# Performance work log

Measured on AMD Instinct MI355X. Metric: run time of the kernel, lower is better.

## Reference

```python
import jax, jax.numpy as jnp
import numpy as np

MAX_STEPS = 50
B, H, A = 4096, 1024, 128


def setup_inputs() -> dict:
    key = jax.random.key(0)
    ks = jax.random.split(key, 7)
    s = 1.0 / np.sqrt(H)  # torch default LSTM/Linear init scale
    return {
        "encoder_output": jax.random.normal(ks[0], (1, B, H), dtype=jnp.float32),
        "w_ih": jax.random.normal(ks[1], (4 * H, H), dtype=jnp.float32) * s,
        "w_hh": jax.random.normal(ks[2], (4 * H, H), dtype=jnp.float32) * s,
        "b_ih": jax.random.normal(ks[3], (4 * H,), dtype=jnp.float32) * s,
        "b_hh": jax.random.normal(ks[4], (4 * H,), dtype=jnp.float32) * s,
        "w_pred": jax.random.normal(ks[5], (A, H), dtype=jnp.float32) * s,
        "b_pred": jax.random.normal(ks[6], (A,), dtype=jnp.float32) * s,
    }


def reference(encoder_output, w_ih, w_hh, b_ih, b_hh, w_pred, b_pred):
    # LSTM output (hidden state) of step t; seq_len is always 1.
    hidden = w_hh.shape[1]
    x0 = encoder_output[0]                        # (B, H)
    h0 = jnp.zeros_like(x0)
    c0 = jnp.zeros_like(x0)
    bias = b_ih + b_hh                            # (4H,)

    def step(carry, _):
        x, h, c = carry
        gates = x @ w_ih.T + h @ w_hh.T + bias    # (B, 4H)
        i, f, g, o = jnp.split(gates, 4, axis=-1)  # torch gate order i,f,g,o
        c_new = jax.nn.sigmoid(f) * c + jax.nn.sigmoid(i) * jnp.tanh(g)
        h_new = jax.nn.sigmoid(o) * jnp.tanh(c_new)
        p = h_new @ w_pred.T + b_pred             # (B, A)
        return (h_new, h_new, c_new), p

    _, predicted = jax.lax.scan(step, (x0, h0, c0), None, length=MAX_STEPS)
    return predicted  # (MAX_STEPS, B, A)
```

## Files before the change

kernel.cpp:

```cpp
#include <hip/hip_runtime.h>
#include <hip/hip_bf16.h>
#include <stdint.h>


#define B_SZ   4096
#define H_SZ   1024
#define A_SZ   128
#define NSTEP  50
#define NT     16

using bf16 = __hip_bfloat16;
typedef __attribute__((ext_vector_type(8))) short bf16x8;
typedef __attribute__((ext_vector_type(4))) float f32x4;

__device__ __forceinline__ void gload_lds16(const void* g, void* l) {
    __builtin_amdgcn_global_load_lds(
        (const __attribute__((address_space(1))) unsigned int*)g,
        (__attribute__((address_space(3))) unsigned int*)l, 16, 0, 0);
}

#define FENCE() asm volatile("" ::: "memory")
#define BAR()   do { FENCE(); __builtin_amdgcn_s_barrier(); FENCE(); } while (0)
#define VMC6()  asm volatile("s_waitcnt vmcnt(6)" ::: "memory")
#define VMC0()  asm volatile("s_waitcnt vmcnt(0)" ::: "memory")
#define LGKM0() asm volatile("s_waitcnt lgkmcnt(0)" ::: "memory")

__device__ __forceinline__ float sigf(float x) {
    return 1.f / (1.f + __expf(-x));
}
__device__ __forceinline__ float tanh_(float x) {
    float e = __expf(-2.f * fabsf(x));
    float t = (1.f - e) / (1.f + e);
    return copysignf(t, x);
}


__global__ void prep_weights(const float4* __restrict__ wih,
                             const float4* __restrict__ whh,
                             bf16* __restrict__ Wc, bf16* __restrict__ Wi) {
    int i = blockIdx.x * 256 + threadIdx.x;
    float4 a = wih[i], b = whh[i];
    bf16 tc[4] = {__float2bfloat16(a.x + b.x), __float2bfloat16(a.y + b.y),
                  __float2bfloat16(a.z + b.z), __float2bfloat16(a.w + b.w)};
    bf16 ti[4] = {__float2bfloat16(a.x), __float2bfloat16(a.y),
                  __float2bfloat16(a.z), __float2bfloat16(a.w)};
    *(uint64_t*)(Wc + 4 * (size_t)i) = *(const uint64_t*)tc;
    *(uint64_t*)(Wi + 4 * (size_t)i) = *(const uint64_t*)ti;
}

__global__ void prep_cast(const float4* __restrict__ in, bf16* __restrict__ out) {
    int i = blockIdx.x * 256 + threadIdx.x;
    float4 a = in[i];
    bf16 t[4] = {__float2bfloat16(a.x), __float2bfloat16(a.y),
                 __float2bfloat16(a.z), __float2bfloat16(a.w)};
    *(uint64_t*)(out + 4 * (size_t)i) = *(const uint64_t*)t;
}

__global__ void prep_bias(const float* __restrict__ a, const float* __restrict__ b,
                          float* __restrict__ o) {
    int i = blockIdx.x * 256 + threadIdx.x;
    o[i] = a[i] + b[i];
}


__global__ __launch_bounds__(512, 2)
void lstm_gates(const bf16* __restrict__ hin, const bf16* __restrict__ W,
                const float* __restrict__ bias, float* __restrict__ c,
                bf16* __restrict__ hout, int step0) {
    __shared__ __align__(16) bf16 sm[65536];
    bf16* const lA0 = sm;
    bf16* const lA1 = sm + 16384;
    bf16* const lB0 = sm + 32768;
    bf16* const lB1 = sm + 49152;

    const int tid  = threadIdx.x;
    const int w    = tid >> 6;
    const int lane = tid & 63;
    const int wr   = w >> 2;
    const int wc   = w & 3;

    const int bid     = blockIdx.x;
    const int logical = (bid & 7) * 32 + (bid >> 3);
    const int bm0     = (logical >> 4) * 256;
    const int j0      = (logical & 15) * 64;

    const int scolb = ((tid & 7) * 16) ^ (((tid >> 3) & 7) << 4);
    const char* baseA = (const char*)hin + (size_t)(bm0 + (tid >> 3)) * 2048 + scolb;
    const char* baseB = (const char*)W   + (size_t)(j0  + (tid >> 3)) * 2048 + scolb;

    const int cs0 = ((      (lane >> 4) * 16) ^ ((lane & 7) << 4)) >> 1;
    const int cs1 = ((64 + (lane >> 4) * 16) ^ ((lane & 7) << 4)) >> 1;
    const int rA  = (wr * 128 + (lane & 15)) * 64;
    const int rB  = (wc * 16  + (lane & 15)) * 64;

    f32x4 acc[8][4];
    const f32x4 z = {0.f, 0.f, 0.f, 0.f};
#pragma unroll
    for (int m = 0; m < 8; ++m)
#pragma unroll
        for (int n = 0; n < 4; ++n) acc[m][n] = z;

    auto SGA = [&](int t, int h) {
        bf16* dst = ((t & 1) ? lA1 : lA0) + h * 8192 + w * 512;
        const char* g = baseA + (size_t)(h * 128) * 2048 + (size_t)t * 128;
        gload_lds16(g, dst);
        gload_lds16(g + (size_t)64 * 2048, dst + 4096);
    };
    auto SGB = [&](int t, int h) {
        bf16* dst = ((t & 1) ? lB1 : lB0) + h * 8192 + w * 512;
        const char* g = baseB + (size_t)(h * 2) * 2097152 + (size_t)t * 128;
        gload_lds16(g, dst);
        gload_lds16(g + 2097152, dst + 4096);
    };

    SGB(0, 0); SGB(0, 1); SGA(0, 0); SGA(0, 1);
    SGB(1, 0); SGB(1, 1); SGA(1, 0);
    VMC6();
    BAR();

    for (int t = 0; t < NT; ++t) {
        const bf16* Ad = (t & 1) ? lA1 : lA0;
        const bf16* Bd = (t & 1) ? lB1 : lB0;
        bf16x8 av[4][2], bv[4][2];

#pragma unroll
        for (int m = 0; m < 4; ++m) {
            av[m][0] = *(const bf16x8*)(Ad + rA + m * 1024 + cs0);
            av[m][1] = *(const bf16x8*)(Ad + rA + m * 1024 + cs1);
        }
#pragma unroll
        for (int n = 0; n < 2; ++n) {
            bv[n][0] = *(const bf16x8*)(Bd + rB + n * 4096 + cs0);
            bv[n][1] = *(const bf16x8*)(Bd + rB + n * 4096 + cs1);
        }
        if (t + 1 < NT) SGA(t + 1, 1);
        BAR(); LGKM0();
        __builtin_amdgcn_s_setprio(1);
#pragma unroll
        for (int n = 0; n < 2; ++n)
#pragma unroll
            for (int m = 0; m < 4; ++m) {
                acc[m][n] = __builtin_amdgcn_mfma_f32_16x16x32_bf16(av[m][0], bv[n][0], acc[m][n], 0, 0, 0);
                acc[m][n] = __builtin_amdgcn_mfma_f32_16x16x32_bf16(av[m][1], bv[n][1], acc[m][n], 0, 0, 0);
            }
        __builtin_amdgcn_s_setprio(0);
        BAR();

#pragma unroll
        for (int n = 2; n < 4; ++n) {
            bv[n][0] = *(const bf16x8*)(Bd + rB + n * 4096 + cs0);
            bv[n][1] = *(const bf16x8*)(Bd + rB + n * 4096 + cs1);
        }
        if (t + 2 < NT) SGB(t + 2, 0);
        BAR(); LGKM0();
        __builtin_amdgcn_s_setprio(1);
#pragma unroll
        for (int n = 2; n < 4; ++n)
#pragma unroll
            for (int m = 0; m < 4; ++m) {
                acc[m][n] = __builtin_amdgcn_mfma_f32_16x16x32_bf16(av[m][0], bv[n][0], acc[m][n], 0, 0, 0);
                acc[m][n] = __builtin_amdgcn_mfma_f32_16x16x32_bf16(av[m][1], bv[n][1], acc[m][n], 0, 0, 0);
            }
        __builtin_amdgcn_s_setprio(0);
        BAR();

#pragma unroll
        for (int m = 0; m < 4; ++m) {
            av[m][0] = *(const bf16x8*)(Ad + rA + (m + 4) * 1024 + cs0);
            av[m][1] = *(const bf16x8*)(Ad + rA + (m + 4) * 1024 + cs1);
        }
        if (t + 2 < NT) SGB(t + 2, 1);
        BAR(); LGKM0();
        __builtin_amdgcn_s_setprio(1);
#pragma unroll
        for (int n = 0; n < 2; ++n)
#pragma unroll
            for (int m = 0; m < 4; ++m) {
                acc[m + 4][n] = __builtin_amdgcn_mfma_f32_16x16x32_bf16(av[m][0], bv[n][0], acc[m + 4][n], 0, 0, 0);
                acc[m + 4][n] = __builtin_amdgcn_mfma_f32_16x16x32_bf16(av[m][1], bv[n][1], acc[m + 4][n], 0, 0, 0);
            }
        __builtin_amdgcn_s_setprio(0);
        BAR();

        if (t + 2 < NT) SGA(t + 2, 0);
        BAR(); LGKM0();
        __builtin_amdgcn_s_setprio(1);
#pragma unroll
        for (int n = 2; n < 4; ++n)
#pragma unroll
            for (int m = 0; m < 4; ++m) {
                acc[m + 4][n] = __builtin_amdgcn_mfma_f32_16x16x32_bf16(av[m][0], bv[n][0], acc[m + 4][n], 0, 0, 0);
                acc[m + 4][n] = __builtin_amdgcn_mfma_f32_16x16x32_bf16(av[m][1], bv[n][1], acc[m + 4][n], 0, 0, 0);
            }
        __builtin_amdgcn_s_setprio(0);
        if (t < NT - 1) {
            if (t == NT - 2) { VMC0(); } else { VMC6(); }
        }
        BAR();
    }

    const int jc = j0 + wc * 16 + (lane & 15);
    const float bi  = bias[jc];
    const float bff = bias[H_SZ + jc];
    const float bg  = bias[2 * H_SZ + jc];
    const float bo  = bias[3 * H_SZ + jc];
#pragma unroll
    for (int m = 0; m < 8; ++m) {
#pragma unroll
        for (int r = 0; r < 4; ++r) {
            int row = bm0 + wr * 128 + m * 16 + (lane >> 4) * 4 + r;
            size_t idx = (size_t)row * H_SZ + jc;
            float iv = acc[m][0][r] + bi;
            float fv = acc[m][1][r] + bff;
            float gv = acc[m][2][r] + bg;
            float ov = acc[m][3][r] + bo;
            float cp = step0 ? 0.f : c[idx];
            float cn = sigf(fv) * cp + sigf(iv) * tanh_(gv);
            float hn = sigf(ov) * tanh_(cn);
            c[idx] = cn;
            hout[idx] = __float2bfloat16(hn);
        }
    }
}


__global__ __launch_bounds__(256)
void pred_kernel(const bf16* __restrict__ h, const bf16* __restrict__ wp,
                 const float* __restrict__ bp, float* __restrict__ out) {
    __shared__ __align__(16) bf16 lH[16 * 64];
    __shared__ __align__(16) bf16 lP[128 * 64];

    const int tid  = threadIdx.x;
    const int w    = tid >> 6;
    const int lane = tid & 63;
    const int bm0  = blockIdx.x * 16;

    const int scolb = ((tid & 7) * 16) ^ (((tid >> 3) & 7) << 4);
    const int cs0 = ((      (lane >> 4) * 16) ^ ((lane & 7) << 4)) >> 1;
    const int cs1 = ((64 + (lane >> 4) * 16) ^ ((lane & 7) << 4)) >> 1;

    f32x4 acc[2];
    const f32x4 z = {0.f, 0.f, 0.f, 0.f};
    acc[0] = z; acc[1] = z;

    const char* hb = (const char*)h  + (size_t)(bm0 + (tid >> 3)) * 2048 + scolb;
    const char* pb = (const char*)wp + (size_t)(tid >> 3) * 2048 + scolb;

    for (int t = 0; t < NT; ++t) {
        __syncthreads();
        if (tid < 128)
            gload_lds16(hb + (size_t)t * 128, lH + w * 512);
#pragma unroll
        for (int q = 0; q < 4; ++q)
            gload_lds16(pb + (size_t)(q * 32) * 2048 + (size_t)t * 128,
                        lP + (q * 4 + w) * 512);
        __syncthreads();

        bf16x8 a0 = *(const bf16x8*)(lH + (lane & 15) * 64 + cs0);
        bf16x8 a1 = *(const bf16x8*)(lH + (lane & 15) * 64 + cs1);
#pragma unroll
        for (int n = 0; n < 2; ++n) {
            int rowb = (w * 32 + n * 16 + (lane & 15)) * 64;
            bf16x8 b0 = *(const bf16x8*)(lP + rowb + cs0);
            bf16x8 b1 = *(const bf16x8*)(lP + rowb + cs1);
            acc[n] = __builtin_amdgcn_mfma_f32_16x16x32_bf16(a0, b0, acc[n], 0, 0, 0);
            acc[n] = __builtin_amdgcn_mfma_f32_16x16x32_bf16(a1, b1, acc[n], 0, 0, 0);
        }
    }

#pragma unroll
    for (int n = 0; n < 2; ++n)
#pragma unroll
        for (int r = 0; r < 4; ++r) {
            int row = bm0 + (lane >> 4) * 4 + r;
            int col = w * 32 + n * 16 + (lane & 15);
            out[(size_t)row * A_SZ + col] = acc[n][r] + bp[col];
        }
}


extern "C" void kernel_launch(void* const* d_in, const int* in_sizes, int n_in,
                              void* d_out, int out_size, void* d_ws, size_t ws_size,
                              hipStream_t stream) {
    const float* enc   = (const float*)d_in[0];
    const float* wih   = (const float*)d_in[1];
    const float* whh   = (const float*)d_in[2];
    const float* bih   = (const float*)d_in[3];
    const float* bhh   = (const float*)d_in[4];
    const float* wpred = (const float*)d_in[5];
    const float* bpred = (const float*)d_in[6];
    float* out = (float*)d_out;

    char* ws = (char*)d_ws;
    const size_t WH = (size_t)4 * H_SZ * H_SZ;
    const size_t BH = (size_t)B_SZ * H_SZ;
    bf16*  Wc   = (bf16*)ws;                 ws += WH * 2;
    bf16*  Wi   = (bf16*)ws;                 ws += WH * 2;
    bf16*  h0   = (bf16*)ws;                 ws += BH * 2;
    bf16*  h1   = (bf16*)ws;                 ws += BH * 2;
    float* cbuf = (float*)ws;                ws += BH * 4;
    bf16*  wp   = (bf16*)ws;                 ws += (size_t)A_SZ * H_SZ * 2;
    float* bias = (float*)ws;                ws += 4 * H_SZ * 4;

    prep_weights<<<4096, 256, 0, stream>>>((const float4*)wih, (const float4*)whh, Wc, Wi);
    prep_cast<<<128, 256, 0, stream>>>((const float4*)wpred, wp);
    prep_bias<<<16, 256, 0, stream>>>(bih, bhh, bias);
    prep_cast<<<4096, 256, 0, stream>>>((const float4*)enc, h0);

    bf16* hbuf[2] = {h0, h1};
    for (int s = 0; s < NSTEP; ++s) {
        const bf16* hin = hbuf[s & 1];
        bf16* hout      = hbuf[(s + 1) & 1];
        lstm_gates<<<256, 512, 0, stream>>>(
            hin, (s == 0) ? Wi : Wc, bias, cbuf, hout, s == 0 ? 1 : 0);
        pred_kernel<<<256, 256, 0, stream>>>(
            hout, wp, bpred, out + (size_t)s * B_SZ * A_SZ);
    }
}
```

Before: 2.671 ms.

## Fuse all LSTM steps and prediction into one persistent cooperative kernel

Replaces the 100 per-step launches (gates kernel plus prediction kernel) with a single cooperative kernel that loops over all 50 steps and uses grid.sync between steps. The cell state now stays in registers instead of being read from and written to global memory every step. The prediction GEMM is folded into the same kernel after the sync and reads h and w_pred straight from global memory. The next step's first tile loads are issued before the prediction work so the two can overlap. In exchange, every step now pays a grid-wide barrier, the whole grid of 256 blocks must be co-resident, and the longer-lived state raises register pressure.

```diff
diff --git a/kernel.cpp b/kernel.cpp
--- a/kernel.cpp
+++ b/kernel.cpp
@@ -1,6 +1,9 @@
 #include <hip/hip_runtime.h>
 #include <hip/hip_bf16.h>
+#include <hip/hip_cooperative_groups.h>
 #include <stdint.h>
+
+namespace cg = cooperative_groups;
 
 
 #define B_SZ   4096
@@ -64,20 +67,24 @@
 
 
 __global__ __launch_bounds__(512, 2)
-void lstm_gates(const bf16* __restrict__ hin, const bf16* __restrict__ W,
-                const float* __restrict__ bias, float* __restrict__ c,
-                bf16* __restrict__ hout, int step0) {
+void lstm_persist(const bf16* __restrict__ Wc, const bf16* __restrict__ Wi,
+                  bf16* __restrict__ hA, bf16* __restrict__ hB,
+                  const float* __restrict__ bias, const bf16* __restrict__ wp,
+                  const float* __restrict__ bp, float* __restrict__ out) {
+    cg::grid_group grid = cg::this_grid();
     __shared__ __align__(16) bf16 sm[65536];
     bf16* const lA0 = sm;
     bf16* const lA1 = sm + 16384;
     bf16* const lB0 = sm + 32768;
     bf16* const lB1 = sm + 49152;
 
-    const int tid  = threadIdx.x;
-    const int w    = tid >> 6;
-    const int lane = tid & 63;
-    const int wr   = w >> 2;
-    const int wc   = w & 3;
+    const int tid    = threadIdx.x;
+    const int w      = tid >> 6;
+    const int lane   = tid & 63;
+    const int wr     = w >> 2;
+    const int wc     = w & 3;
+    const int lane15 = lane & 15;
+    const int lhi    = lane >> 4;
 
     const int bid     = blockIdx.x;
     const int logical = (bid & 7) * 32 + (bid >> 3);
@@ -85,197 +92,181 @@
     const int j0      = (logical & 15) * 64;
 
     const int scolb = ((tid & 7) * 16) ^ (((tid >> 3) & 7) << 4);
-    const char* baseA = (const char*)hin + (size_t)(bm0 + (tid >> 3)) * 2048 + scolb;
-    const char* baseB = (const char*)W   + (size_t)(j0  + (tid >> 3)) * 2048 + scolb;
-
-    const int cs0 = ((      (lane >> 4) * 16) ^ ((lane & 7) << 4)) >> 1;
-    const int cs1 = ((64 + (lane >> 4) * 16) ^ ((lane & 7) << 4)) >> 1;
-    const int rA  = (wr * 128 + (lane & 15)) * 64;
-    const int rB  = (wc * 16  + (lane & 15)) * 64;
-
-    f32x4 acc[8][4];
-    const f32x4 z = {0.f, 0.f, 0.f, 0.f};
+    const size_t offA = (size_t)(bm0 + (tid >> 3)) * 2048 + scolb;
+    const size_t offB = (size_t)(j0  + (tid >> 3)) * 2048 + scolb;
+
+    const int cs0 = ((     lhi * 16) ^ ((lane & 7) << 4)) >> 1;
+    const int cs1 = ((64 + lhi * 16) ^ ((lane & 7) << 4)) >> 1;
+    const int rA  = (wr * 128 + lane15) * 64;
+    const int rB  = (wc * 16  + lane15) * 64;
+
+    const int jc = j0 + wc * 16 + lane15;
+    const float bi  = bias[jc];
+    const float bff = bias[H_SZ + jc];
+    const float bg  = bias[2 * H_SZ + jc];
+    const float bo  = bias[3 * H_SZ + jc];
+    const float bpv = bp[w * 16 + lane15];
+    const int pr0 = logical * 16;
+
+    float creg[8][4];
 #pragma unroll
     for (int m = 0; m < 8; ++m)
 #pragma unroll
-        for (int n = 0; n < 4; ++n) acc[m][n] = z;
+        for (int r = 0; r < 4; ++r) creg[m][r] = 0.f;
+
+    const char* gA = (const char*)hA + offA;
+    const char* gB = (const char*)Wi + offB;
 
     auto SGA = [&](int t, int h) {
         bf16* dst = ((t & 1) ? lA1 : lA0) + h * 8192 + w * 512;
-        const char* g = baseA + (size_t)(h * 128) * 2048 + (size_t)t * 128;
+        const char* g = gA + (size_t)(h * 128) * 2048 + (size_t)t * 128;
         gload_lds16(g, dst);
         gload_lds16(g + (size_t)64 * 2048, dst + 4096);
     };
     auto SGB = [&](int t, int h) {
         bf16* dst = ((t & 1) ? lB1 : lB0) + h * 8192 + w * 512;
-        const char* g = baseB + (size_t)(h * 2) * 2097152 + (size_t)t * 128;
+        const char* g = gB + (size_t)(h * 2) * 2097152 + (size_t)t * 128;
         gload_lds16(g, dst);
         gload_lds16(g + 2097152, dst + 4096);
     };
 
     SGB(0, 0); SGB(0, 1); SGA(0, 0); SGA(0, 1);
     SGB(1, 0); SGB(1, 1); SGA(1, 0);
-    VMC6();
-    BAR();
-
-    for (int t = 0; t < NT; ++t) {
-        const bf16* Ad = (t & 1) ? lA1 : lA0;
-        const bf16* Bd = (t & 1) ? lB1 : lB0;
-        bf16x8 av[4][2], bv[4][2];
-
-#pragma unroll
-        for (int m = 0; m < 4; ++m) {
-            av[m][0] = *(const bf16x8*)(Ad + rA + m * 1024 + cs0);
-            av[m][1] = *(const bf16x8*)(Ad + rA + m * 1024 + cs1);
+
+    const f32x4 z = {0.f, 0.f, 0.f, 0.f};
+
+    for (int s = 0; s < NSTEP; ++s) {
+        bf16* hnew = (s & 1) ? hA : hB;
+
+        VMC6();
+        BAR();
+
+        f32x4 acc[8][4];
+#pragma unroll
+        for (int m = 0; m < 8; ++m)
+#pragma unroll
+            for (int n = 0; n < 4; ++n) acc[m][n] = z;
+
+        for (int t = 0; t < NT; ++t) {
+            const bf16* Ad = (t & 1) ? lA1 : lA0;
+            const bf16* Bd = (t & 1) ? lB1 : lB0;
+            bf16x8 av[4][2], bv[4][2];
+
+#pragma unroll
+            for (int m = 0; m < 4; ++m) {
+                av[m][0] = *(const bf16x8*)(Ad + rA + m * 1024 + cs0);
+                av[m][1] = *(const bf16x8*)(Ad + rA + m * 1024 + cs1);
+            }
+#pragma unroll
+            for (int n = 0; n < 2; ++n) {
+                bv[n][0] = *(const bf16x8*)(Bd + rB + n * 4096 + cs0);
+                bv[n][1] = *(const bf16x8*)(Bd + rB + n * 4096 + cs1);
+            }
+            if (t + 1 < NT) SGA(t + 1, 1);
+            BAR(); LGKM0();
+            __builtin_amdgcn_s_setprio(1);
+#pragma unroll
+            for (int n = 0; n < 2; ++n)
+#pragma unroll
+                for (int m = 0; m < 4; ++m) {
+                    acc[m][n] = __builtin_amdgcn_mfma_f32_16x16x32_bf16(av[m][0], bv[n][0], acc[m][n], 0, 0, 0);
+                    acc[m][n] = __builtin_amdgcn_mfma_f32_16x16x32_bf16(av[m][1], bv[n][1], acc[m][n], 0, 0, 0);
+                }
+            __builtin_amdgcn_s_setprio(0);
+            BAR();
+
+#pragma unroll
+            for (int n = 2; n < 4; ++n) {
+                bv[n][0] = *(const bf16x8*)(Bd + rB + n * 4096 + cs0);
+                bv[n][1] = *(const bf16x8*)(Bd + rB + n * 4096 + cs1);
+            }
+            if (t + 2 < NT) SGB(t + 2, 0);
+            BAR(); LGKM0();
+            __builtin_amdgcn_s_setprio(1);
+#pragma unroll
+            for (int n = 2; n < 4; ++n)
+#pragma unroll
+                for (int m = 0; m < 4; ++m) {
+                    acc[m][n] = __builtin_amdgcn_mfma_f32_16x16x32_bf16(av[m][0], bv[n][0], acc[m][n], 0, 0, 0);
+                    acc[m][n] = __builtin_amdgcn_mfma_f32_16x16x32_bf16(av[m][1], bv[n][1], acc[m][n], 0, 0, 0);
+                }
+            __builtin_amdgcn_s_setprio(0);
+            BAR();
+
+#pragma unroll
+            for (int m = 0; m < 4; ++m) {
+                av[m][0] = *(const bf16x8*)(Ad + rA + (m + 4) * 1024 + cs0);
+                av[m][1] = *(const bf16x8*)(Ad + rA + (m + 4) * 1024 + cs1);
+            }
+            if (t + 2 < NT) SGB(t + 2, 1);
+            BAR(); LGKM0();
+            __builtin_amdgcn_s_setprio(1);
+#pragma unroll
+            for (int n = 0; n < 2; ++n)
+#pragma unroll
+                for (int m = 0; m < 4; ++m) {
+                    acc[m + 4][n] = __builtin_amdgcn_mfma_f32_16x16x32_bf16(av[m][0], bv[n][0], acc[m + 4][n], 0, 0, 0);
+                    acc[m + 4][n] = __builtin_amdgcn_mfma_f32_16x16x32_bf16(av[m][1], bv[n][1], acc[m + 4][n], 0, 0, 0);
+                }
+            __builtin_amdgcn_s_setprio(0);
+            BAR();
+
+            if (t + 2 < NT) SGA(t + 2, 0);
+            BAR(); LGKM0();
+            __builtin_amdgcn_s_setprio(1);
+#pragma unroll
+            for (int n = 2; n < 4; ++n)
+#pragma unroll
+                for (int m = 0; m < 4; ++m) {
+                    acc[m + 4][n] = __builtin_amdgcn_mfma_f32_16x16x32_bf16(av[m][0], bv[n][0], acc[m + 4][n], 0, 0, 0);
+                    acc[m + 4][n] = __builtin_amdgcn_mfma_f32_16x16x32_bf16(av[m][1], bv[n][1], acc[m + 4][n], 0, 0, 0);
+                }
+            __builtin_amdgcn_s_setprio(0);
+            if (t < NT - 1) {
+                if (t == NT - 2) { VMC0(); } else { VMC6(); }
+            }
+            BAR();
         }
-#pragma unroll
-        for (int n = 0; n < 2; ++n) {
-            bv[n][0] = *(const bf16x8*)(Bd + rB + n * 4096 + cs0);
-            bv[n][1] = *(const bf16x8*)(Bd + rB + n * 4096 + cs1);
+
+#pragma unroll
+        for (int m = 0; m < 8; ++m) {
+#pragma unroll
+            for (int r = 0; r < 4; ++r) {
+                int row = bm0 + wr * 128 + m * 16 + lhi * 4 + r;
+                float iv = acc[m][0][r] + bi;
+                float fv = acc[m][1][r] + bff;
+                float gv = acc[m][2][r] + bg;
+                float ov = acc[m][3][r] + bo;
+                float cn = sigf(fv) * creg[m][r] + sigf(iv) * tanh_(gv);
+                float hn = sigf(ov) * tanh_(cn);
+                creg[m][r] = cn;
+                hnew[(size_t)row * H_SZ + jc] = __float2bfloat16(hn);
+            }
         }
-        if (t + 1 < NT) SGA(t + 1, 1);
-        BAR(); LGKM0();
-        __builtin_amdgcn_s_setprio(1);
-#pragma unroll
-        for (int n = 0; n < 2; ++n)
-#pragma unroll
-            for (int m = 0; m < 4; ++m) {
-                acc[m][n] = __builtin_amdgcn_mfma_f32_16x16x32_bf16(av[m][0], bv[n][0], acc[m][n], 0, 0, 0);
-                acc[m][n] = __builtin_amdgcn_mfma_f32_16x16x32_bf16(av[m][1], bv[n][1], acc[m][n], 0, 0, 0);
-            }
-        __builtin_amdgcn_s_setprio(0);
-        BAR();
-
-#pragma unroll
-        for (int n = 2; n < 4; ++n) {
-            bv[n][0] = *(const bf16x8*)(Bd + rB + n * 4096 + cs0);
-            bv[n][1] = *(const bf16x8*)(Bd + rB + n * 4096 + cs1);
+
+        grid.sync();
+
+        if (s + 1 < NSTEP) {
+            gA = (const char*)hnew + offA;
+            gB = (const char*)Wc + offB;
+            SGB(0, 0); SGB(0, 1); SGA(0, 0); SGA(0, 1);
+            SGB(1, 0); SGB(1, 1); SGA(1, 0);
         }
-        if (t + 2 < NT) SGB(t + 2, 0);
-        BAR(); LGKM0();
-        __builtin_amdgcn_s_setprio(1);
-#pragma unroll
-        for (int n = 2; n < 4; ++n)
-#pragma unroll
-            for (int m = 0; m < 4; ++m) {
-                acc[m][n] = __builtin_amdgcn_mfma_f32_16x16x32_bf16(av[m][0], bv[n][0], acc[m][n], 0, 0, 0);
-                acc[m][n] = __builtin_amdgcn_mfma_f32_16x16x32_bf16(av[m][1], bv[n][1], acc[m][n], 0, 0, 0);
-            }
-        __builtin_amdgcn_s_setprio(0);
-        BAR();
-
-#pragma unroll
-        for (int m = 0; m < 4; ++m) {
-            av[m][0] = *(const bf16x8*)(Ad + rA + (m + 4) * 1024 + cs0);
-            av[m][1] = *(const bf16x8*)(Ad + rA + (m + 4) * 1024 + cs1);
+
+        const bf16* hp  = hnew + (size_t)(pr0 + lane15) * H_SZ + lhi * 8;
+        const bf16* wpp = wp   + (size_t)(w * 16 + lane15) * H_SZ + lhi * 8;
+        f32x4 pacc = z;
+#pragma unroll 4
+        for (int ks = 0; ks < 32; ++ks) {
+            bf16x8 a = *(const bf16x8*)(hp + ks * 32);
+            bf16x8 b = *(const bf16x8*)(wpp + ks * 32);
+            pacc = __builtin_amdgcn_mfma_f32_16x16x32_bf16(a, b, pacc, 0, 0, 0);
         }
-        if (t + 2 < NT) SGB(t + 2, 1);
-        BAR(); LGKM0();
-        __builtin_amdgcn_s_setprio(1);
-#pragma unroll
-        for (int n = 0; n < 2; ++n)
-#pragma unroll
-            for (int m = 0; m < 4; ++m) {
-                acc[m + 4][n] = __builtin_amdgcn_mfma_f32_16x16x32_bf16(av[m][0], bv[n][0], acc[m + 4][n], 0, 0, 0);
-                acc[m + 4][n] = __builtin_amdgcn_mfma_f32_16x16x32_bf16(av[m][1], bv[n][1], acc[m + 4][n], 0, 0, 0);
-            }
-        __builtin_amdgcn_s_setprio(0);
-        BAR();
-
-        if (t + 2 < NT) SGA(t + 2, 0);
-        BAR(); LGKM0();
-        __builtin_amdgcn_s_setprio(1);
-#pragma unroll
-        for (int n = 2; n < 4; ++n)
-#pragma unroll
-            for (int m = 0; m < 4; ++m) {
-                acc[m + 4][n] = __builtin_amdgcn_mfma_f32_16x16x32_bf16(av[m][0], bv[n][0], acc[m + 4][n], 0, 0, 0);
-                acc[m + 4][n] = __builtin_amdgcn_mfma_f32_16x16x32_bf16(av[m][1], bv[n][1], acc[m + 4][n], 0, 0, 0);
-            }
-        __builtin_amdgcn_s_setprio(0);
-        if (t < NT - 1) {
-            if (t == NT - 2) { VMC0(); } else { VMC6(); }
-        }
-        BAR();
+        float* op = out + (size_t)s * (B_SZ * A_SZ)
+                  + (size_t)(pr0 + lhi * 4) * A_SZ + w * 16 + lane15;
+#pragma unroll
+        for (int r = 0; r < 4; ++r) op[r * A_SZ] = pacc[r] + bpv;
     }
-
-    const int jc = j0 + wc * 16 + (lane & 15);
-    const float bi  = bias[jc];
-    const float bff = bias[H_SZ + jc];
-    const float bg  = bias[2 * H_SZ + jc];
-    const float bo  = bias[3 * H_SZ + jc];
-#pragma unroll
-    for (int m = 0; m < 8; ++m) {
-#pragma unroll
-        for (int r = 0; r < 4; ++r) {
-            int row = bm0 + wr * 128 + m * 16 + (lane >> 4) * 4 + r;
-            size_t idx = (size_t)row * H_SZ + jc;
-            float iv = acc[m][0][r] + bi;
-            float fv = acc[m][1][r] + bff;
-            float gv = acc[m][2][r] + bg;
-            float ov = acc[m][3][r] + bo;
-            float cp = step0 ? 0.f : c[idx];
-            float cn = sigf(fv) * cp + sigf(iv) * tanh_(gv);
-            float hn = sigf(ov) * tanh_(cn);
-            c[idx] = cn;
-            hout[idx] = __float2bfloat16(hn);
-        }
-    }
-}
-
-
-__global__ __launch_bounds__(256)
-void pred_kernel(const bf16* __restrict__ h, const bf16* __restrict__ wp,
-                 const float* __restrict__ bp, float* __restrict__ out) {
-    __shared__ __align__(16) bf16 lH[16 * 64];
-    __shared__ __align__(16) bf16 lP[128 * 64];
-
-    const int tid  = threadIdx.x;
-    const int w    = tid >> 6;
-    const int lane = tid & 63;
-    const int bm0  = blockIdx.x * 16;
-
-    const int scolb = ((tid & 7) * 16) ^ (((tid >> 3) & 7) << 4);
-    const int cs0 = ((      (lane >> 4) * 16) ^ ((lane & 7) << 4)) >> 1;
-    const int cs1 = ((64 + (lane >> 4) * 16) ^ ((lane & 7) << 4)) >> 1;
-
-    f32x4 acc[2];
-    const f32x4 z = {0.f, 0.f, 0.f, 0.f};
-    acc[0] = z; acc[1] = z;
-
-    const char* hb = (const char*)h  + (size_t)(bm0 + (tid >> 3)) * 2048 + scolb;
-    const char* pb = (const char*)wp + (size_t)(tid >> 3) * 2048 + scolb;
-
-    for (int t = 0; t < NT; ++t) {
-        __syncthreads();
-        if (tid < 128)
-            gload_lds16(hb + (size_t)t * 128, lH + w * 512);
-#pragma unroll
-        for (int q = 0; q < 4; ++q)
-            gload_lds16(pb + (size_t)(q * 32) * 2048 + (size_t)t * 128,
-                        lP + (q * 4 + w) * 512);
-        __syncthreads();
-
-        bf16x8 a0 = *(const bf16x8*)(lH + (lane & 15) * 64 + cs0);
-        bf16x8 a1 = *(const bf16x8*)(lH + (lane & 15) * 64 + cs1);
-#pragma unroll
-        for (int n = 0; n < 2; ++n) {
-            int rowb = (w * 32 + n * 16 + (lane & 15)) * 64;
-            bf16x8 b0 = *(const bf16x8*)(lP + rowb + cs0);
-            bf16x8 b1 = *(const bf16x8*)(lP + rowb + cs1);
-            acc[n] = __builtin_amdgcn_mfma_f32_16x16x32_bf16(a0, b0, acc[n], 0, 0, 0);
-            acc[n] = __builtin_amdgcn_mfma_f32_16x16x32_bf16(a1, b1, acc[n], 0, 0, 0);
-        }
-    }
-
-#pragma unroll
-    for (int n = 0; n < 2; ++n)
-#pragma unroll
-        for (int r = 0; r < 4; ++r) {
-            int row = bm0 + (lane >> 4) * 4 + r;
-            int col = w * 32 + n * 16 + (lane & 15);
-            out[(size_t)row * A_SZ + col] = acc[n][r] + bp[col];
-        }
 }
 
 
@@ -298,7 +289,6 @@
     bf16*  Wi   = (bf16*)ws;                 ws += WH * 2;
     bf16*  h0   = (bf16*)ws;                 ws += BH * 2;
     bf16*  h1   = (bf16*)ws;                 ws += BH * 2;
-    float* cbuf = (float*)ws;                ws += BH * 4;
     bf16*  wp   = (bf16*)ws;                 ws += (size_t)A_SZ * H_SZ * 2;
     float* bias = (float*)ws;                ws += 4 * H_SZ * 4;
 
@@ -307,13 +297,8 @@
     prep_bias<<<16, 256, 0, stream>>>(bih, bhh, bias);
     prep_cast<<<4096, 256, 0, stream>>>((const float4*)enc, h0);
 
-    bf16* hbuf[2] = {h0, h1};
-    for (int s = 0; s < NSTEP; ++s) {
-        const bf16* hin = hbuf[s & 1];
-        bf16* hout      = hbuf[(s + 1) & 1];
-        lstm_gates<<<256, 512, 0, stream>>>(
-            hin, (s == 0) ? Wi : Wc, bias, cbuf, hout, s == 0 ? 1 : 0);
-        pred_kernel<<<256, 256, 0, stream>>>(
-            hout, wp, bpred, out + (size_t)s * B_SZ * A_SZ);
-    }
-}
+    void* args[] = {(void*)&Wc, (void*)&Wi, (void*)&h0, (void*)&h1,
+                    (void*)&bias, (void*)&wp, (void*)&bpred, (void*)&out};
+    hipLaunchCooperativeKernel((const void*)lstm_persist, dim3(256), dim3(512),
+                               args, 0, stream);
+}
```

Result: slower. 4.479 ms (+67.7%).

## Fuse prediction projection of previous step into next LSTM gates kernel

Applied to the files above, without the earlier changes.

The per-step prediction kernel is removed. Each lstm_gates launch now computes the output projection for the previous step's hidden state (its input hin) in its prologue, overlapping with the initial async LDS loads, and a single pred_kernel handles the final step. This halves the number of kernel launches and reuses the hidden-state read, at the cost of extra prologue work and register pressure in the gates kernel.

```diff
diff --git a/kernel.cpp b/kernel.cpp
--- a/kernel.cpp
+++ b/kernel.cpp
@@ -66,18 +66,22 @@
 __global__ __launch_bounds__(512, 2)
 void lstm_gates(const bf16* __restrict__ hin, const bf16* __restrict__ W,
                 const float* __restrict__ bias, float* __restrict__ c,
-                bf16* __restrict__ hout, int step0) {
+                bf16* __restrict__ hout, int step0,
+                const bf16* __restrict__ wp, const float* __restrict__ bp,
+                float* __restrict__ pout) {
     __shared__ __align__(16) bf16 sm[65536];
     bf16* const lA0 = sm;
     bf16* const lA1 = sm + 16384;
     bf16* const lB0 = sm + 32768;
     bf16* const lB1 = sm + 49152;
 
-    const int tid  = threadIdx.x;
-    const int w    = tid >> 6;
-    const int lane = tid & 63;
-    const int wr   = w >> 2;
-    const int wc   = w & 3;
+    const int tid    = threadIdx.x;
+    const int w      = tid >> 6;
+    const int lane   = tid & 63;
+    const int wr     = w >> 2;
+    const int wc     = w & 3;
+    const int lane15 = lane & 15;
+    const int lhi    = lane >> 4;
 
     const int bid     = blockIdx.x;
     const int logical = (bid & 7) * 32 + (bid >> 3);
@@ -88,10 +92,10 @@
     const char* baseA = (const char*)hin + (size_t)(bm0 + (tid >> 3)) * 2048 + scolb;
     const char* baseB = (const char*)W   + (size_t)(j0  + (tid >> 3)) * 2048 + scolb;
 
-    const int cs0 = ((      (lane >> 4) * 16) ^ ((lane & 7) << 4)) >> 1;
-    const int cs1 = ((64 + (lane >> 4) * 16) ^ ((lane & 7) << 4)) >> 1;
-    const int rA  = (wr * 128 + (lane & 15)) * 64;
-    const int rB  = (wc * 16  + (lane & 15)) * 64;
+    const int cs0 = ((     lhi * 16) ^ ((lane & 7) << 4)) >> 1;
+    const int cs1 = ((64 + lhi * 16) ^ ((lane & 7) << 4)) >> 1;
+    const int rA  = (wr * 128 + lane15) * 64;
+    const int rB  = (wc * 16  + lane15) * 64;
 
     f32x4 acc[8][4];
     const f32x4 z = {0.f, 0.f, 0.f, 0.f};
@@ -115,6 +119,24 @@
 
     SGB(0, 0); SGB(0, 1); SGA(0, 0); SGA(0, 1);
     SGB(1, 0); SGB(1, 1); SGA(1, 0);
+
+    if (pout) {
+        const int pr0 = logical * 16;
+        const bf16* hp  = hin + (size_t)(pr0 + lane15) * H_SZ + lhi * 8;
+        const bf16* wpp = wp  + (size_t)(w * 16 + lane15) * H_SZ + lhi * 8;
+        f32x4 pacc = z;
+#pragma unroll 4
+        for (int ks = 0; ks < 32; ++ks) {
+            bf16x8 a = *(const bf16x8*)(hp + ks * 32);
+            bf16x8 b = *(const bf16x8*)(wpp + ks * 32);
+            pacc = __builtin_amdgcn_mfma_f32_16x16x32_bf16(a, b, pacc, 0, 0, 0);
+        }
+        const float bpv = bp[w * 16 + lane15];
+        float* op = pout + (size_t)(pr0 + lhi * 4) * A_SZ + w * 16 + lane15;
+#pragma unroll
+        for (int r = 0; r < 4; ++r) op[r * A_SZ] = pacc[r] + bpv;
+    }
+
     VMC6();
     BAR();
 
@@ -199,7 +221,7 @@
         BAR();
     }
 
-    const int jc = j0 + wc * 16 + (lane & 15);
+    const int jc = j0 + wc * 16 + lane15;
     const float bi  = bias[jc];
     const float bff = bias[H_SZ + jc];
     const float bg  = bias[2 * H_SZ + jc];
@@ -208,7 +230,7 @@
     for (int m = 0; m < 8; ++m) {
 #pragma unroll
         for (int r = 0; r < 4; ++r) {
-            int row = bm0 + wr * 128 + m * 16 + (lane >> 4) * 4 + r;
+            int row = bm0 + wr * 128 + m * 16 + lhi * 4 + r;
             size_t idx = (size_t)row * H_SZ + jc;
             float iv = acc[m][0][r] + bi;
             float fv = acc[m][1][r] + bff;
@@ -311,9 +333,11 @@
     for (int s = 0; s < NSTEP; ++s) {
         const bf16* hin = hbuf[s & 1];
         bf16* hout      = hbuf[(s + 1) & 1];
+        float* pout = (s == 0) ? nullptr : out + (size_t)(s - 1) * (B_SZ * A_SZ);
         lstm_gates<<<256, 512, 0, stream>>>(
-            hin, (s == 0) ? Wi : Wc, bias, cbuf, hout, s == 0 ? 1 : 0);
-        pred_kernel<<<256, 256, 0, stream>>>(
-            hout, wp, bpred, out + (size_t)s * B_SZ * A_SZ);
-    }
-}
+            hin, (s == 0) ? Wi : Wc, bias, cbuf, hout, s == 0 ? 1 : 0,
+            wp, bpred, pout);
+    }
+    pred_kernel<<<256, 256, 0, stream>>>(
+        hbuf[0], wp, bpred, out + (size_t)(NSTEP - 1) * (B_SZ * A_SZ));
+}
```

Result: slower. 2.819 ms (+5.5%).
